# Performance work log

Hardware: AMD Instinct MI355X
Metric: run time of the kernel (lower is better)

The kernel has to match this reference:

```python
import jax, jax.numpy as jnp
import numpy as np
from jax import lax

B = 128      # graphs per batch
N = 68       # facial landmarks (num_nodes per graph)
C = 3        # input channels
P = 32       # PATCH_SIZE
K = 16       # NUM_KERNELS
FD = 64      # feature_dim
GH = 128     # gcn_hidden_dim
OUT = 2      # output_dim
EG = 8 * N   # edges per graph
T = B * N    # total nodes


def setup_inputs() -> dict:
    key = jax.random.key(0)
    ks = jax.random.split(key, 8)
    x = jax.random.normal(ks[0], (T, C, P, P), jnp.float32)
    e = jax.random.randint(ks[1], (2, B, EG), 0, N)
    offs = (jnp.arange(B) * N)[None, :, None]
    edge_index = (e + offs).reshape(2, -1)            # within-graph edges, global ids
    batch = jnp.repeat(jnp.arange(B), N)              # node -> graph id
    conv_w = jax.random.normal(ks[2], (N, K, C, 3, 3), jnp.float32) * 0.05
    conv_b = jnp.zeros((N, K), jnp.float32)
    lin1_w = jax.random.normal(ks[3], (N, K * (P // 2) * (P // 2), FD), jnp.float32) * 0.02
    lin1_b = jnp.zeros((N, FD), jnp.float32)
    gcn_w = jax.random.normal(ks[4], (FD, GH), jnp.float32) * 0.1
    gcn_b = jnp.zeros((GH,), jnp.float32)
    mlp_w1 = jax.random.normal(ks[5], (GH, GH // 2), jnp.float32) * 0.1
    mlp_b1 = jnp.zeros((GH // 2,), jnp.float32)
    mlp_w2 = jax.random.normal(ks[6], (GH // 2, OUT), jnp.float32) * 0.1
    mlp_b2 = jnp.zeros((OUT,), jnp.float32)
    return dict(x=x, edge_index=edge_index, batch=batch, conv_w=conv_w, conv_b=conv_b,
                lin1_w=lin1_w, lin1_b=lin1_b, gcn_w=gcn_w, gcn_b=gcn_b,
                mlp_w1=mlp_w1, mlp_b1=mlp_b1, mlp_w2=mlp_w2, mlp_b2=mlp_b2)


def reference(x, edge_index, batch, conv_w, conv_b, lin1_w, lin1_b,
              gcn_w, gcn_b, mlp_w1, mlp_b1, mlp_w2, mlp_b2):
    # --- per-node-type CNN routing (nodes are laid out [graph, local_index]) ---
    xr = x.reshape(B, N, C, P, P)

    def cnn_one(xn, w, b):           # xn: [B,C,P,P]  w: [K,C,3,3]
        y = lax.conv_general_dilated(xn, w, (1, 1), 'SAME',
                                     dimension_numbers=('NCHW', 'OIHW', 'NCHW'))
        return jax.nn.relu(y + b[None, :, None, None])

    a = jax.vmap(cnn_one, in_axes=(1, 0, 0), out_axes=1)(xr, conv_w, conv_b)  # [B,N,K,P,P]
    pooled = lax.reduce_window(a, -jnp.inf, lax.max,
                               (1, 1, 1, 2, 2), (1, 1, 1, 2, 2), 'VALID')     # [B,N,K,P/2,P/2]
    flat = pooled.reshape(B, N, -1)
    feats = jax.nn.relu(jnp.einsum('bnf,nfo->bno', flat, lin1_w) + lin1_b[None])  # [B,N,FD]
    nodes = feats.reshape(T, FD)

    # --- GCNConv: add self-loops, symmetric normalization ---
    loop = jnp.arange(T)
    src = jnp.concatenate([edge_index[0], loop])
    dst = jnp.concatenate([edge_index[1], loop])
    deg = jax.ops.segment_sum(jnp.ones_like(dst, jnp.float32), dst, T)
    dis = jnp.where(deg > 0, 1.0 / jnp.sqrt(deg), 0.0)
    norm = dis[src] * dis[dst]
    xw = nodes @ gcn_w                                   # [T,GH]
    h = jax.ops.segment_sum(norm[:, None] * xw[src], dst, T) + gcn_b
    h = jax.nn.relu(h)

    # --- global mean pool over graphs ---
    cnt = jax.ops.segment_sum(jnp.ones((T,), jnp.float32), batch, B)
    g = jax.ops.segment_sum(h, batch, B) / cnt[:, None]  # [B,GH]

    # --- MLP head ---
    z = jax.nn.relu(g @ mlp_w1 + mlp_b1)
    return z @ mlp_w2 + mlp_b2                           # [B,OUT]
```

## Files before the change

kernel.cpp:

```cpp
#include <hip/hip_runtime.h>
#include <hip/hip_fp16.h>

#define B_   128
#define N_   68
#define C_   3
#define P_   32
#define K_   16
#define FD_  64
#define GH_  128
#define EG_  544
#define T_   8704
#define FLAT_ 4096
#define FCH_ 16

typedef __attribute__((ext_vector_type(8))) _Float16 half8;
typedef __attribute__((ext_vector_type(2))) _Float16 half2v;
typedef __attribute__((ext_vector_type(4))) float   floatx4;
typedef __attribute__((ext_vector_type(4))) unsigned int uint32x4;

#define ROWP 40
#define CHP  1400

__global__ __launch_bounds__(256) void wfrag_prep_kernel(
    const float* __restrict__ conv_w, _Float16* __restrict__ wfrag) {
  const int n = blockIdx.x;
  const int tid = threadIdx.x;
  const float* wp = conv_w + (size_t)n * (K_ * 27);
  _Float16* out = wfrag + (size_t)n * 2048;
  for (int i = tid; i < 2048; i += 256) {
    int sx   = (i >> 10) & 1;
    int type = (i >> 9) & 1;
    int k    = (i >> 5) & 15;
    int slot = i & 31;
    float v = 0.0f;
    if (type == 0) {
      int q = slot >> 3, r = (slot >> 2) & 1, col = slot & 3;
      int cr = q * 2 + r, c = cr / 3, dy = cr - c * 3, dx = col - sx;
      if (dx >= 0 && dx < 3) v = wp[k * 27 + c * 9 + dy * 3 + dx];
    } else {
      int q = slot >> 3, j = slot & 7;
      if (q == 0 && j < 4) {
        int dx = j - sx;
        if (dx >= 0 && dx < 3) v = wp[k * 27 + 24 + dx];
      }
    }
    out[i] = (_Float16)v;
  }
}

__global__ __launch_bounds__(256) void conv_pool_kernel(
    const float* __restrict__ x, const _Float16* __restrict__ wfrag,
    const float* __restrict__ conv_b, _Float16* __restrict__ pooled) {
  const int t = blockIdx.x;
  const int n = t % N_;
  const int tid = threadIdx.x;

  __shared__ _Float16 xsh[3 * CHP];

  const int lane = tid & 63;
  const int lr = lane & 15, q = lane >> 4;
  const int wave = tid >> 6;
  const int ldy = lr >> 3, ldx = lr & 7;

  const float4* xg = (const float4*)(x + (size_t)t * (C_ * P_ * P_));
  float4 xv[3];
  #pragma unroll
  for (int j = 0; j < 3; j++) xv[j] = xg[tid + j * 256];

  const _Float16* wf = wfrag + (size_t)n * 2048 + lr * 32 + q * 8;
  half8 aMain0 = *(const half8*)&wf[0 * 512];
  half8 aCorr0 = *(const half8*)&wf[1 * 512];
  half8 aMain1 = *(const half8*)&wf[2 * 512];
  half8 aCorr1 = *(const half8*)&wf[3 * 512];
  floatx4 cbias = *(const floatx4*)&conv_b[(size_t)n * K_ + q * 4];

  for (int i = tid; i < 396; i += 256) {
    int c = i / 132, j = i - c * 132;
    int off;
    if (j < 34)       off = j;
    else if (j < 68)  off = 33 * ROWP + (j - 34);
    else if (j < 100) off = (j - 68 + 1) * ROWP;
    else              off = (j - 100 + 1) * ROWP + 33;
    xsh[c * CHP + off] = (_Float16)0.0f;
  }
  #pragma unroll
  for (int j = 0; j < 3; j++) {
    int f0 = (tid + j * 256) * 4;
    int c = f0 >> 10, rem = f0 & 1023, y = rem >> 5, xc = rem & 31;
    _Float16* dp = &xsh[c * CHP + (y + 1) * ROWP + xc + 1];
    dp[0] = (_Float16)xv[j].x; dp[1] = (_Float16)xv[j].y;
    dp[2] = (_Float16)xv[j].z; dp[3] = (_Float16)xv[j].w;
  }
  __syncthreads();

  const int crL = q * 2, crH = crL + 1;
  const int cL = crL / 3, dyL = crL - cL * 3;
  const int cH = crH / 3, dyH = crH - cH * 3;
  const _Float16* chL = &xsh[cL * CHP + dyL * ROWP];
  const _Float16* chH = &xsh[cH * CHP + dyH * ROWP];
  const _Float16* chC = &xsh[2 * CHP + 2 * ROWP];

  #pragma unroll
  for (int i = 0; i < 4; i++) {
    const int qq = wave * 4 + i;
    const int py0 = (qq >> 1) * 2, px0 = (qq & 1) * 8;
    const int py = py0 + ldy, px = px0 + ldx;
    const int ebase = py * (2 * ROWP) + px * 2;
    const _Float16* pL = chL + ebase;
    const _Float16* pH = chH + ebase;
    const _Float16* pC = chC + ebase;

    floatx4 mx;
    #pragma unroll
    for (int sy = 0; sy < 2; sy++) {
      unsigned int uL0 = *(const unsigned int*)&pL[sy * ROWP];
      unsigned int uL1 = *(const unsigned int*)&pL[sy * ROWP + 2];
      unsigned int uH0 = *(const unsigned int*)&pH[sy * ROWP];
      unsigned int uH1 = *(const unsigned int*)&pH[sy * ROWP + 2];
      unsigned int uC0 = *(const unsigned int*)&pC[sy * ROWP];
      unsigned int uC1 = *(const unsigned int*)&pC[sy * ROWP + 2];
      half8 bMain = __builtin_bit_cast(half8, (uint32x4){uL0, uL1, uH0, uH1});
      half8 bCorr = __builtin_bit_cast(half8, (uint32x4){uC0, uC1, uC0, uC1});
      floatx4 d0 = __builtin_amdgcn_mfma_f32_16x16x32_f16(aCorr0, bCorr, cbias, 0, 0, 0);
      d0 = __builtin_amdgcn_mfma_f32_16x16x32_f16(aMain0, bMain, d0, 0, 0, 0);
      floatx4 d1 = __builtin_amdgcn_mfma_f32_16x16x32_f16(aCorr1, bCorr, cbias, 0, 0, 0);
      d1 = __builtin_amdgcn_mfma_f32_16x16x32_f16(aMain1, bMain, d1, 0, 0, 0);
      floatx4 m;
      m[0] = fmaxf(d0[0], d1[0]); m[1] = fmaxf(d0[1], d1[1]);
      m[2] = fmaxf(d0[2], d1[2]); m[3] = fmaxf(d0[3], d1[3]);
      if (sy == 0) mx = m;
      else {
        mx[0] = fmaxf(mx[0], m[0]); mx[1] = fmaxf(mx[1], m[1]);
        mx[2] = fmaxf(mx[2], m[2]); mx[3] = fmaxf(mx[3], m[3]);
      }
    }
    _Float16* op = pooled + (size_t)t * FLAT_ + q * 1024 + py * 16 + px;
    op[0]   = (_Float16)fmaxf(mx[0], 0.0f);
    op[256] = (_Float16)fmaxf(mx[1], 0.0f);
    op[512] = (_Float16)fmaxf(mx[2], 0.0f);
    op[768] = (_Float16)fmaxf(mx[3], 0.0f);
  }
}

__global__ __launch_bounds__(256) void lin1_mfma_kernel(
    const _Float16* __restrict__ pooled, const float* __restrict__ lin1_w,
    float* __restrict__ part) {
  const int n   = blockIdx.x >> 4;
  const int fc  = blockIdx.x & 15;
  const int tid = threadIdx.x;
  const int wave = tid >> 6, lane = tid & 63;
  const int q = lane >> 4, lr = lane & 15;

  __shared__ __align__(16) _Float16 As[128 * 72];
  __shared__ __align__(16) _Float16 Bt[64 * 72];

  floatx4 acc[2][4];
  #pragma unroll
  for (int mt = 0; mt < 2; mt++)
    #pragma unroll
    for (int nt = 0; nt < 4; nt++)
      acc[mt][nt] = (floatx4){0.f, 0.f, 0.f, 0.f};

  const int f_base = fc * 256;
  for (int step = 0; step < 4; step++) {
    const int f0 = f_base + step * 64;

    #pragma unroll
    for (int j = 0; j < 4; j++) {
      int idx = tid + j * 256;
      int r = idx >> 3, ch = idx & 7;
      uint4 v = *(const uint4*)&pooled[(size_t)(r * N_ + n) * FLAT_ + f0 + ch * 8];
      *(uint4*)&As[r * 72 + ch * 8] = v;
    }
    const float* wg = &lin1_w[(size_t)n * (FLAT_ * FD_) + (size_t)f0 * FD_];
    #pragma unroll
    for (int it = 0; it < 2; it++) {
      int p = tid + it * 256;
      int o0 = (p & 15) * 4, k0 = (p >> 4) * 2;
      const float* wgk = wg + k0 * 64 + o0;
      float4 va = *(const float4*)wgk;
      float4 vb = *(const float4*)(wgk + 64);
      *(half2v*)&Bt[(o0 + 0) * 72 + k0] = (half2v){(_Float16)va.x, (_Float16)vb.x};
      *(half2v*)&Bt[(o0 + 1) * 72 + k0] = (half2v){(_Float16)va.y, (_Float16)vb.y};
      *(half2v*)&Bt[(o0 + 2) * 72 + k0] = (half2v){(_Float16)va.z, (_Float16)vb.z};
      *(half2v*)&Bt[(o0 + 3) * 72 + k0] = (half2v){(_Float16)va.w, (_Float16)vb.w};
    }
    __syncthreads();

    #pragma unroll
    for (int kh = 0; kh < 2; kh++) {
      half8 af[2], bf[4];
      #pragma unroll
      for (int mt = 0; mt < 2; mt++)
        af[mt] = *(const half8*)&As[(wave * 32 + mt * 16 + lr) * 72 + kh * 32 + q * 8];
      #pragma unroll
      for (int nt = 0; nt < 4; nt++)
        bf[nt] = *(const half8*)&Bt[(nt * 16 + lr) * 72 + kh * 32 + q * 8];
      #pragma unroll
      for (int mt = 0; mt < 2; mt++)
        #pragma unroll
        for (int nt = 0; nt < 4; nt++)
          acc[mt][nt] = __builtin_amdgcn_mfma_f32_16x16x32_f16(
              af[mt], bf[nt], acc[mt][nt], 0, 0, 0);
    }
    __syncthreads();
  }

  float* pb = part + (size_t)fc * T_ * FD_;
  #pragma unroll
  for (int mt = 0; mt < 2; mt++) {
    #pragma unroll
    for (int v = 0; v < 4; v++) {
      int r = wave * 32 + mt * 16 + q * 4 + v;
      size_t base = (size_t)(r * N_ + n) * FD_;
      #pragma unroll
      for (int nt = 0; nt < 4; nt++)
        pb[base + nt * 16 + lr] = acc[mt][nt][v];
    }
  }
}

__global__ __launch_bounds__(256) void feats_kernel(
    const float* __restrict__ part, const float* __restrict__ lin1_b,
    float* __restrict__ feats) {
  int gid = blockIdx.x * 256 + threadIdx.x;
  int t = gid >> 4, f4 = (gid & 15) * 4;
  int n = t % N_;
  float4 s = *(const float4*)&lin1_b[n * FD_ + f4];
  #pragma unroll
  for (int fc = 0; fc < FCH_; fc++) {
    float4 v = *(const float4*)&part[((size_t)fc * T_ + t) * FD_ + f4];
    s.x += v.x; s.y += v.y; s.z += v.z; s.w += v.w;
  }
  s.x = fmaxf(s.x, 0.f); s.y = fmaxf(s.y, 0.f);
  s.z = fmaxf(s.z, 0.f); s.w = fmaxf(s.w, 0.f);
  *(float4*)&feats[(size_t)t * FD_ + f4] = s;
}

__global__ __launch_bounds__(256) void gcn_agg_kernel(
    const float* __restrict__ feats, const int* __restrict__ edge_index,
    float* __restrict__ agg) {
  const int b  = blockIdx.x >> 1;
  const int fh = blockIdx.x & 1;
  const int tid = threadIdx.x;

  __shared__ float fS[N_ * 33], aS[N_ * 33];
  __shared__ int   esrcS[EG_], edstS[EG_];
  __shared__ float nrmS[EG_];
  __shared__ int   degS[N_];
  __shared__ float disS[N_];

  if (tid < N_) degS[tid] = 0;
  const int* srcp = edge_index;
  const int* dstp = edge_index + (B_ * EG_);
  const int e0 = b * EG_, nbase = b * N_;
  for (int e = tid; e < EG_; e += 256) {
    esrcS[e] = srcp[e0 + e] - nbase;
    edstS[e] = dstp[e0 + e] - nbase;
  }
  for (int idx = tid; idx < N_ * 32; idx += 256) {
    int i = idx >> 5, f = idx & 31;
    fS[i * 33 + f] = feats[(size_t)(b * N_ + i) * FD_ + fh * 32 + f];
  }
  __syncthreads();
  for (int e = tid; e < EG_; e += 256) atomicAdd(&degS[edstS[e]], 1);
  __syncthreads();
  if (tid < N_) disS[tid] = rsqrtf((float)(degS[tid] + 1));
  __syncthreads();
  for (int e = tid; e < EG_; e += 256)
    nrmS[e] = disS[esrcS[e]] * disS[edstS[e]];
  for (int idx = tid; idx < N_ * 32; idx += 256) {
    int i = idx >> 5, f = idx & 31;
    float d = disS[i];
    aS[i * 33 + f] = d * d * fS[i * 33 + f];
  }
  __syncthreads();
  for (int idx = tid; idx < EG_ * 32; idx += 256) {
    int e = idx >> 5, f = idx & 31;
    atomicAdd(&aS[edstS[e] * 33 + f], nrmS[e] * fS[esrcS[e] * 33 + f]);
  }
  __syncthreads();
  for (int idx = tid; idx < N_ * 32; idx += 256) {
    int i = idx >> 5, f = idx & 31;
    agg[(size_t)(b * N_ + i) * FD_ + fh * 32 + f] = aS[i * 33 + f];
  }
}

__global__ __launch_bounds__(512) void gcn_head_kernel(
    const float* __restrict__ agg, const float* __restrict__ gcn_w,
    const float* __restrict__ gcn_b, const float* __restrict__ w1,
    const float* __restrict__ b1, const float* __restrict__ w2,
    const float* __restrict__ b2, float* __restrict__ out) {
  const int b = blockIdx.x;
  const int tid = threadIdx.x;

  __shared__ float aS[N_ * 68];
  __shared__ float wS[FD_ * GH_];
  __shared__ float gP[4][GH_];
  __shared__ float z1S[64];

  for (int i4 = tid; i4 < N_ * 16; i4 += 512) {
    int i = i4 >> 4, qf = (i4 & 15) * 4;
    *(float4*)&aS[i * 68 + qf] = *(const float4*)&agg[(size_t)(b * N_ + i) * FD_ + qf];
  }
  #pragma unroll
  for (int j = 0; j < 4; j++)
    ((float4*)wS)[tid + j * 512] = ((const float4*)gcn_w)[tid + j * 512];
  __syncthreads();

  const int j = tid & 127, ig = tid >> 7;
  float wc[64];
  #pragma unroll
  for (int k = 0; k < 64; k++) wc[k] = wS[k * GH_ + j];
  const float bias = gcn_b[j];
  float gsum = 0.f;
  for (int i = ig; i < N_; i += 4) {
    float acc = bias;
    #pragma unroll
    for (int kq = 0; kq < 16; kq++) {
      float4 a = *(const float4*)&aS[i * 68 + kq * 4];
      acc += a.x * wc[kq * 4] + a.y * wc[kq * 4 + 1]
           + a.z * wc[kq * 4 + 2] + a.w * wc[kq * 4 + 3];
    }
    gsum += fmaxf(acc, 0.f);
  }
  gP[ig][j] = gsum;
  __syncthreads();
  if (tid < GH_)
    gP[0][tid] = (gP[0][tid] + gP[1][tid] + gP[2][tid] + gP[3][tid]) * (1.f / 68.f);
  __syncthreads();
  if (tid < 64) {
    float s = b1[tid];
    #pragma unroll 8
    for (int jj = 0; jj < GH_; jj++) s += gP[0][jj] * w1[jj * 64 + tid];
    z1S[tid] = fmaxf(s, 0.f);
  }
  __syncthreads();
  if (tid < 2) {
    float s = b2[tid];
    #pragma unroll 8
    for (int jj = 0; jj < 64; jj++) s += z1S[jj] * w2[jj * 2 + tid];
    out[b * 2 + tid] = s;
  }
}

extern "C" void kernel_launch(void* const* d_in, const int* in_sizes, int n_in,
                              void* d_out, int out_size, void* d_ws, size_t ws_size,
                              hipStream_t stream) {
  const float* x        = (const float*)d_in[0];
  const int*   edge_idx = (const int*)d_in[1];
  const float* conv_w   = (const float*)d_in[3];
  const float* conv_b   = (const float*)d_in[4];
  const float* lin1_w   = (const float*)d_in[5];
  const float* lin1_b   = (const float*)d_in[6];
  const float* gcn_w    = (const float*)d_in[7];
  const float* gcn_b    = (const float*)d_in[8];
  const float* mlp_w1   = (const float*)d_in[9];
  const float* mlp_b1   = (const float*)d_in[10];
  const float* mlp_w2   = (const float*)d_in[11];
  const float* mlp_b2   = (const float*)d_in[12];
  float* outp = (float*)d_out;

  char* wsb = (char*)d_ws;
  _Float16* pooled = (_Float16*)wsb;
  float* part  = (float*)(wsb + (size_t)T_ * FLAT_ * 2);
  float* feats = part + (size_t)FCH_ * T_ * FD_;
  float* agg   = feats + (size_t)T_ * FD_;
  _Float16* wfrag = (_Float16*)(agg + (size_t)T_ * FD_);

  wfrag_prep_kernel<<<N_, 256, 0, stream>>>(conv_w, wfrag);
  conv_pool_kernel<<<T_, 256, 0, stream>>>(x, wfrag, conv_b, pooled);
  lin1_mfma_kernel<<<N_ * FCH_, 256, 0, stream>>>(pooled, lin1_w, part);
  feats_kernel<<<544, 256, 0, stream>>>(part, lin1_b, feats);
  gcn_agg_kernel<<<B_ * 2, 256, 0, stream>>>(feats, edge_idx, agg);
  gcn_head_kernel<<<B_, 512, 0, stream>>>(agg, gcn_w, gcn_b,
                                          mlp_w1, mlp_b1, mlp_w2, mlp_b2, outp);
}
```

Measured before the change: 311.8 us.

## Store pooled features position-major with vector writes and halve lin1 partial sums

```diff
diff --git a/kernel.cpp b/kernel.cpp
--- a/kernel.cpp
+++ b/kernel.cpp
@@ -14,12 +14,14 @@
 #define FCH_ 16
 
 typedef __attribute__((ext_vector_type(8))) _Float16 half8;
+typedef __attribute__((ext_vector_type(4))) _Float16 half4v;
 typedef __attribute__((ext_vector_type(2))) _Float16 half2v;
 typedef __attribute__((ext_vector_type(4))) float   floatx4;
 typedef __attribute__((ext_vector_type(4))) unsigned int uint32x4;
 
 #define ROWP 40
 #define CHP  1400
+
 
 __global__ __launch_bounds__(256) void wfrag_prep_kernel(
     const float* __restrict__ conv_w, _Float16* __restrict__ wfrag) {
@@ -134,17 +136,18 @@
         mx[2] = fmaxf(mx[2], m[2]); mx[3] = fmaxf(mx[3], m[3]);
       }
     }
-    _Float16* op = pooled + (size_t)t * FLAT_ + q * 1024 + py * 16 + px;
-    op[0]   = (_Float16)fmaxf(mx[0], 0.0f);
-    op[256] = (_Float16)fmaxf(mx[1], 0.0f);
-    op[512] = (_Float16)fmaxf(mx[2], 0.0f);
-    op[768] = (_Float16)fmaxf(mx[3], 0.0f);
+    half4v hv;
+    hv[0] = (_Float16)fmaxf(mx[0], 0.0f);
+    hv[1] = (_Float16)fmaxf(mx[1], 0.0f);
+    hv[2] = (_Float16)fmaxf(mx[2], 0.0f);
+    hv[3] = (_Float16)fmaxf(mx[3], 0.0f);
+    *(half4v*)(pooled + (size_t)t * FLAT_ + (py * 16 + px) * 16 + q * 4) = hv;
   }
 }
 
 __global__ __launch_bounds__(256) void lin1_mfma_kernel(
     const _Float16* __restrict__ pooled, const float* __restrict__ lin1_w,
-    float* __restrict__ part) {
+    _Float16* __restrict__ part) {
   const int n   = blockIdx.x >> 4;
   const int fc  = blockIdx.x & 15;
   const int tid = threadIdx.x;
@@ -162,6 +165,8 @@
       acc[mt][nt] = (floatx4){0.f, 0.f, 0.f, 0.f};
 
   const int f_base = fc * 256;
+  const float* wg = &lin1_w[(size_t)n * (FLAT_ * FD_)];
+
   for (int step = 0; step < 4; step++) {
     const int f0 = f_base + step * 64;
 
@@ -172,14 +177,15 @@
       uint4 v = *(const uint4*)&pooled[(size_t)(r * N_ + n) * FLAT_ + f0 + ch * 8];
       *(uint4*)&As[r * 72 + ch * 8] = v;
     }
-    const float* wg = &lin1_w[(size_t)n * (FLAT_ * FD_) + (size_t)f0 * FD_];
     #pragma unroll
     for (int it = 0; it < 2; it++) {
       int p = tid + it * 256;
       int o0 = (p & 15) * 4, k0 = (p >> 4) * 2;
-      const float* wgk = wg + k0 * 64 + o0;
+      int kch = k0 & 15;
+      int s   = fc * 16 + step * 4 + (k0 >> 4);
+      const float* wgk = wg + ((size_t)(kch * 256 + s)) * FD_ + o0;
       float4 va = *(const float4*)wgk;
-      float4 vb = *(const float4*)(wgk + 64);
+      float4 vb = *(const float4*)(wgk + 256 * FD_);
       *(half2v*)&Bt[(o0 + 0) * 72 + k0] = (half2v){(_Float16)va.x, (_Float16)vb.x};
       *(half2v*)&Bt[(o0 + 1) * 72 + k0] = (half2v){(_Float16)va.y, (_Float16)vb.y};
       *(half2v*)&Bt[(o0 + 2) * 72 + k0] = (half2v){(_Float16)va.z, (_Float16)vb.z};
@@ -206,31 +212,32 @@
     __syncthreads();
   }
 
-  float* pb = part + (size_t)fc * T_ * FD_;
   #pragma unroll
   for (int mt = 0; mt < 2; mt++) {
     #pragma unroll
     for (int v = 0; v < 4; v++) {
       int r = wave * 32 + mt * 16 + q * 4 + v;
-      size_t base = (size_t)(r * N_ + n) * FD_;
+      size_t base = ((size_t)(r * N_ + n) * FCH_ + fc) * FD_;
       #pragma unroll
       for (int nt = 0; nt < 4; nt++)
-        pb[base + nt * 16 + lr] = acc[mt][nt][v];
+        part[base + nt * 16 + lr] = (_Float16)acc[mt][nt][v];
     }
   }
 }
 
 __global__ __launch_bounds__(256) void feats_kernel(
-    const float* __restrict__ part, const float* __restrict__ lin1_b,
+    const _Float16* __restrict__ part, const float* __restrict__ lin1_b,
     float* __restrict__ feats) {
   int gid = blockIdx.x * 256 + threadIdx.x;
   int t = gid >> 4, f4 = (gid & 15) * 4;
   int n = t % N_;
+  const _Float16* pp = &part[(size_t)t * FCH_ * FD_ + f4];
   float4 s = *(const float4*)&lin1_b[n * FD_ + f4];
   #pragma unroll
   for (int fc = 0; fc < FCH_; fc++) {
-    float4 v = *(const float4*)&part[((size_t)fc * T_ + t) * FD_ + f4];
-    s.x += v.x; s.y += v.y; s.z += v.z; s.w += v.w;
+    half4v v = *(const half4v*)&pp[fc * FD_];
+    s.x += (float)v[0]; s.y += (float)v[1];
+    s.z += (float)v[2]; s.w += (float)v[3];
   }
   s.x = fmaxf(s.x, 0.f); s.y = fmaxf(s.y, 0.f);
   s.z = fmaxf(s.z, 0.f); s.w = fmaxf(s.w, 0.f);
@@ -363,10 +370,10 @@
 
   char* wsb = (char*)d_ws;
   _Float16* pooled = (_Float16*)wsb;
-  float* part  = (float*)(wsb + (size_t)T_ * FLAT_ * 2);
-  float* feats = part + (size_t)FCH_ * T_ * FD_;
-  float* agg   = feats + (size_t)T_ * FD_;
-  _Float16* wfrag = (_Float16*)(agg + (size_t)T_ * FD_);
+  _Float16* part   = pooled + (size_t)T_ * FLAT_;
+  float* feats     = (float*)(part + (size_t)T_ * FCH_ * FD_);
+  float* agg       = feats + (size_t)T_ * FD_;
+  _Float16* wfrag  = (_Float16*)(agg + (size_t)T_ * FD_);
 
   wfrag_prep_kernel<<<N_, 256, 0, stream>>>(conv_w, wfrag);
   conv_pool_kernel<<<T_, 256, 0, stream>>>(x, wfrag, conv_b, pooled);
```

After: 305.3 us. 2.1% less time.
